# Kernel tuning notes

Hardware: AMD Instinct MI355X
Metric: run time of the kernel (lower is better)

## Reference

```python
import jax, jax.numpy as jnp
import numpy as np

B, N, D, H, L = 1024, 500, 128, 8, 2  # batch, nb_nodes, dim_emb, nb_heads, nb_layers_decoder
CLIP = 10.0


def _mha(q, K, V, h, mask, clip):
    # q: (B,1,D) single query; K,V: (B,N,D); mask: (B,N) True = forbidden
    Bsz, Nn, Dd = K.shape
    dh = Dd // h
    qh = q.reshape(Bsz, h, dh)            # head k takes contiguous chunk of dim_emb (matches torch view)
    Kh = K.reshape(Bsz, Nn, h, dh)
    Vh = V.reshape(Bsz, Nn, h, dh)
    scores = jnp.einsum('bhd,bnhd->bhn', qh, Kh) / jnp.sqrt(jnp.asarray(dh, q.dtype))
    if clip is not None:
        scores = clip * jnp.tanh(scores)
    scores = jnp.where(mask[:, None, :], jnp.asarray(-1e9, scores.dtype), scores)
    w = jax.nn.softmax(scores, axis=-1)   # (B,h,N)
    out = jnp.einsum('bhn,bnhd->bhd', w, Vh).reshape(Bsz, 1, Dd)
    return out, w.mean(axis=1, keepdims=True)  # (B,1,D), (B,1,N)


def setup_inputs() -> dict:
    key = jax.random.key(0)
    ks = jax.random.split(key, 8)
    query = jax.random.normal(ks[0], (B, 1, D), dtype=jnp.float32)
    K_att = jax.random.normal(ks[1], (B, N, D * L), dtype=jnp.float32)
    V_att = jax.random.normal(ks[2], (B, N, D * L), dtype=jnp.float32)
    mask = jax.random.bernoulli(ks[3], 0.3, (B, N))
    mask = mask.at[:, 0].set(False)  # guarantee every row has a legal action
    s = 1.0 / np.sqrt(D)
    W0_w = jax.random.normal(ks[4], (D, D), dtype=jnp.float32) * s
    W0_b = jnp.zeros((D,), dtype=jnp.float32)
    Wq_w = jax.random.normal(ks[5], (D, D), dtype=jnp.float32) * s
    Wq_b = jnp.zeros((D,), dtype=jnp.float32)
    return {"query": query, "K_att": K_att, "V_att": V_att, "mask": mask,
            "W0_w": W0_w, "W0_b": W0_b, "Wq_w": Wq_w, "Wq_b": Wq_b}


def reference(query, K_att, V_att, mask, W0_w, W0_b, Wq_w, Wq_b):
    q = query
    attn_w = None
    for l in range(L):
        Kl = K_att[:, :, l * D:(l + 1) * D]
        Vl = V_att[:, :, l * D:(l + 1) * D]
        if l < L - 1:
            out, _ = _mha(q, Kl, Vl, H, mask, None)
            q = out @ W0_w.T + W0_b
        else:
            qf = q @ Wq_w.T + Wq_b
            _, attn_w = _mha(qf, Kl, Vl, 1, mask, CLIP)
    return attn_w[:, 0, :]  # (B, N) prob of next node
```

## Files before the change

kernel.cpp:

```cpp
#include <hip/hip_runtime.h>
#include <hip/hip_bf16.h>
#include <math.h>

constexpr int NKEY = 500;
constexpr int DIM = 128;
constexpr int ROWSTRIDE = 256;

typedef __attribute__((ext_vector_type(4))) float f32x4;

__device__ __forceinline__ f32x4 nt_load4(const float* p) {
    return __builtin_nontemporal_load((const f32x4*)p);
}
__device__ __forceinline__ void nt_store(float* p, float v) {
    __builtin_nontemporal_store(v, p);
}
__device__ __forceinline__ float fast_tanh10(float x) {
    const float ax = fabsf(x);
    const float e = __expf(2.f * ax);
    const float r = 1.f - 2.f / (e + 1.f);
    return copysignf(10.f * r, x);
}

__global__ __launch_bounds__(256, 5)
void fused_pomo_attn(const float* __restrict__ query,
                     const float* __restrict__ K_att,
                     const float* __restrict__ V_att,
                     const int*   __restrict__ mask,
                     const float* __restrict__ W0_w,
                     const float* __restrict__ W0_b,
                     const float* __restrict__ Wq_w,
                     const float* __restrict__ Wq_b,
                     float* __restrict__ out)
{
    const int b = blockIdx.x;
    const int tid = threadIdx.x;
    const int lane32 = tid & 31;
    const int grp = tid >> 5;

    __shared__ alignas(16) float s_red[8][DIM];
    __shared__ float s_m8[8][32];
    __shared__ float s_l8[8][32];
    __shared__ alignas(16) float s_out[DIM];
    __shared__ alignas(16) float s_q1[DIM];
    __shared__ alignas(16) float s_qf[DIM];
    __shared__ alignas(16) float s_s1[NKEY];
    __shared__ int s_idx[NKEY];
    __shared__ int s_cnt;
    __shared__ float s_m[4], s_l[4];

    const size_t brow = (size_t)b * NKEY;

    if (tid < 64) {
        int off = 0;
        for (int base = 0; base < NKEY; base += 64) {
            const int n = base + tid;
            const bool keep = (n < NKEY) && (mask[brow + n] == 0);
            const unsigned long long bal = __ballot(keep);
            const int pre = __popcll(bal & ((1ull << tid) - 1ull));
            if (keep) s_idx[off + pre] = n;
            off += __popcll(bal);
        }
        if (tid == 0) s_cnt = off;
    }
    __syncthreads();
    const int M = s_cnt;
    const int Mm1 = M - 1;

    {
        const f32x4 q4 = ((const f32x4*)(query + (size_t)b * DIM))[lane32];
        const float* Kb = K_att + brow * ROWSTRIDE + lane32 * 4;
        const float* Vb = V_att + brow * ROWSTRIDE + lane32 * 4;
        float m = -1e30f, l = 0.f;
        f32x4 acc; acc[0]=0.f; acc[1]=0.f; acc[2]=0.f; acc[3]=0.f;
        for (int base = 0; base < M; base += 32) {
            int n[4]; bool okv[4];
            #pragma unroll
            for (int j = 0; j < 4; j++) {
                const int p = base + 8*j + grp;
                okv[j] = p < M;
                n[j] = s_idx[okv[j] ? p : Mm1];
            }
            f32x4 k[4], v[4];
            #pragma unroll
            for (int j = 0; j < 4; j++) k[j] = nt_load4(Kb + (size_t)n[j] * ROWSTRIDE);
            #pragma unroll
            for (int j = 0; j < 4; j++) v[j] = nt_load4(Vb + (size_t)n[j] * ROWSTRIDE);
            float s[4];
            #pragma unroll
            for (int j = 0; j < 4; j++)
                s[j] = q4[0]*k[j][0] + q4[1]*k[j][1] + q4[2]*k[j][2] + q4[3]*k[j][3];
            #pragma unroll
            for (int j = 0; j < 4; j++) { s[j] += __shfl_xor(s[j], 1); s[j] += __shfl_xor(s[j], 2); }
            #pragma unroll
            for (int j = 0; j < 4; j++) s[j] = okv[j] ? s[j] * 0.25f : -1e30f;
            float m2 = m;
            #pragma unroll
            for (int j = 0; j < 4; j++) m2 = fmaxf(m2, s[j]);
            const float f = __expf(m - m2);
            float w[4];
            #pragma unroll
            for (int j = 0; j < 4; j++) w[j] = __expf(s[j] - m2);
            l = l * f + (w[0] + w[1]) + (w[2] + w[3]);
            #pragma unroll
            for (int d = 0; d < 4; d++) {
                float a = acc[d] * f;
                #pragma unroll
                for (int j = 0; j < 4; j++) a += w[j] * v[j][d];
                acc[d] = a;
            }
            m = m2;
        }
        ((f32x4*)s_red[grp])[lane32] = acc;
        s_m8[grp][lane32] = m;
        s_l8[grp][lane32] = l;
    }
    __syncthreads();
    if (tid < DIM) {
        const int ql = tid >> 2;
        float M_ = -1e30f;
        #pragma unroll
        for (int g = 0; g < 8; g++) M_ = fmaxf(M_, s_m8[g][ql]);
        float L = 0.f, o = 0.f;
        #pragma unroll
        for (int g = 0; g < 8; g++) {
            const float f = __expf(s_m8[g][ql] - M_);
            L += s_l8[g][ql] * f;
            o += s_red[g][tid] * f;
        }
        s_out[tid] = o / L;
    }
    __syncthreads();

    {
        const int i = tid >> 1, half = tid & 1;
        const float4* wrow = (const float4*)(W0_w + (size_t)i * DIM + half * 64);
        float ssum = 0.f;
        #pragma unroll
        for (int k = 0; k < 16; k++) {
            const float4 w4 = wrow[k];
            const float4 o4 = ((const float4*)s_out)[half * 16 + k];
            ssum += w4.x*o4.x + w4.y*o4.y + w4.z*o4.z + w4.w*o4.w;
        }
        ssum += __shfl_xor(ssum, 1);
        if (half == 0) s_q1[i] = ssum + W0_b[i];
    }
    __syncthreads();

    {
        const int i = tid >> 1, half = tid & 1;
        const float4* wrow = (const float4*)(Wq_w + (size_t)i * DIM + half * 64);
        float ssum = 0.f;
        #pragma unroll
        for (int k = 0; k < 16; k++) {
            const float4 w4 = wrow[k];
            const float4 o4 = ((const float4*)s_q1)[half * 16 + k];
            ssum += w4.x*o4.x + w4.y*o4.y + w4.z*o4.z + w4.w*o4.w;
        }
        ssum += __shfl_xor(ssum, 1);
        if (half == 0) s_qf[i] = ssum + Wq_b[i];
    }
    __syncthreads();

    {
        const f32x4 qf4 = ((const f32x4*)s_qf)[lane32];
        const float* K1b = K_att + brow * ROWSTRIDE + DIM + lane32 * 4;
        f32x4 kt[4];
        #pragma unroll
        for (int j = 0; j < 4; j++) {
            const int p = 8*j + grp;
            const int nn = s_idx[p < M ? p : Mm1];
            kt[j] = nt_load4(K1b + (size_t)nn * ROWSTRIDE);
        }
        for (int base = 0; base < M; base += 32) {
            f32x4 kn[4];
            #pragma unroll
            for (int j = 0; j < 4; j++) {
                const int p = base + 32 + 8*j + grp;
                const int nn = s_idx[p < M ? p : Mm1];
                kn[j] = nt_load4(K1b + (size_t)nn * ROWSTRIDE);
            }
            float s[4];
            #pragma unroll
            for (int j = 0; j < 4; j++)
                s[j] = qf4[0]*kt[j][0] + qf4[1]*kt[j][1] + qf4[2]*kt[j][2] + qf4[3]*kt[j][3];
            #pragma unroll
            for (int o = 1; o < 32; o <<= 1) {
                #pragma unroll
                for (int j = 0; j < 4; j++) s[j] += __shfl_xor(s[j], o);
            }
            if (lane32 == 0) {
                #pragma unroll
                for (int j = 0; j < 4; j++) {
                    const int p = base + 8*j + grp;
                    if (p < M) s_s1[p] = fast_tanh10(s[j] * 0.08838834764831845f);
                }
            }
            #pragma unroll
            for (int j = 0; j < 4; j++) kt[j] = kn[j];
        }
    }
    for (int n = tid; n < NKEY; n += 256) nt_store(out + brow + n, 0.f);
    __syncthreads();

    {
        const int wid = tid >> 6;
        const int lane = tid & 63;
        float m = -INFINITY;
        for (int p = tid; p < M; p += 256) m = fmaxf(m, s_s1[p]);
        #pragma unroll
        for (int o = 32; o > 0; o >>= 1) m = fmaxf(m, __shfl_xor(m, o));
        if (lane == 0) s_m[wid] = m;
        __syncthreads();
        m = fmaxf(fmaxf(s_m[0], s_m[1]), fmaxf(s_m[2], s_m[3]));
        float l = 0.f;
        for (int p = tid; p < M; p += 256) {
            const float e = __expf(s_s1[p] - m);
            s_s1[p] = e;
            l += e;
        }
        #pragma unroll
        for (int o = 32; o > 0; o >>= 1) l += __shfl_xor(l, o);
        if (lane == 0) s_l[wid] = l;
        __syncthreads();
        l = s_l[0] + s_l[1] + s_l[2] + s_l[3];
        const float inv = 1.f / l;
        for (int p = tid; p < M; p += 256) nt_store(out + brow + s_idx[p], s_s1[p] * inv);
    }
}

extern "C" void kernel_launch(void* const* d_in, const int* in_sizes, int n_in,
                              void* d_out, int out_size, void* d_ws, size_t ws_size,
                              hipStream_t stream) {
    const float* query = (const float*)d_in[0];
    const float* K_att = (const float*)d_in[1];
    const float* V_att = (const float*)d_in[2];
    const int*   mask  = (const int*)d_in[3];
    const float* W0_w  = (const float*)d_in[4];
    const float* W0_b  = (const float*)d_in[5];
    const float* Wq_w  = (const float*)d_in[6];
    const float* Wq_b  = (const float*)d_in[7];
    float* out = (float*)d_out;

    const int B = in_sizes[0] / DIM;
    fused_pomo_attn<<<B, 256, 0, stream>>>(query, K_att, V_att, mask,
                                           W0_w, W0_b, Wq_w, Wq_b, out);
}
```

Before: 104.8 us.

## Parallelize mask compaction across waves and prefetch layer-1 keys earlier

Mask compaction now runs across all four waves, using per-wave ballot counts and a prefix sum instead of one wave looping eight times. The first 64 gathered K rows of the second layer are loaded right after the first attention pass, so their latency overlaps the reduction and the two small matvecs. The score loop now prefetches two tiles ahead. Holding the extra prefetch registers required lowering the occupancy hint from 5 to 4 blocks per SM, which reduces latency hiding across blocks.

Result: no change. 106.1 us (+1.2%).

```diff
diff --git a/kernel.cpp b/kernel.cpp
--- a/kernel.cpp
+++ b/kernel.cpp
@@ -21,7 +21,7 @@
     return copysignf(10.f * r, x);
 }
 
-__global__ __launch_bounds__(256, 5)
+__global__ __launch_bounds__(256, 4)
 void fused_pomo_attn(const float* __restrict__ query,
                      const float* __restrict__ K_att,
                      const float* __restrict__ V_att,
@@ -45,25 +45,34 @@
     __shared__ alignas(16) float s_qf[DIM];
     __shared__ alignas(16) float s_s1[NKEY];
     __shared__ int s_idx[NKEY];
-    __shared__ int s_cnt;
+    __shared__ int s_wcnt[4];
     __shared__ float s_m[4], s_l[4];
 
     const size_t brow = (size_t)b * NKEY;
 
-    if (tid < 64) {
-        int off = 0;
-        for (int base = 0; base < NKEY; base += 64) {
-            const int n = base + tid;
-            const bool keep = (n < NKEY) && (mask[brow + n] == 0);
-            const unsigned long long bal = __ballot(keep);
-            const int pre = __popcll(bal & ((1ull << tid) - 1ull));
-            if (keep) s_idx[off + pre] = n;
-            off += __popcll(bal);
-        }
-        if (tid == 0) s_cnt = off;
-    }
-    __syncthreads();
-    const int M = s_cnt;
+    {
+        const int cwid = tid >> 6;
+        const int cwl  = tid & 63;
+        const int kstart = cwid * 128;
+        const int kend   = min(kstart + 128, NKEY);
+        const int n0 = kstart + cwl;
+        const int n1 = kstart + 64 + cwl;
+        const bool keep0 = (n0 < kend) && (mask[brow + n0] == 0);
+        const bool keep1 = (n1 < kend) && (mask[brow + n1] == 0);
+        const unsigned long long b0 = __ballot(keep0);
+        const unsigned long long b1 = __ballot(keep1);
+        const int c0 = __popcll(b0);
+        if (cwl == 0) s_wcnt[cwid] = c0 + __popcll(b1);
+        __syncthreads();
+        int pref = 0;
+        #pragma unroll
+        for (int w = 0; w < 4; w++) if (w < cwid) pref += s_wcnt[w];
+        const unsigned long long mlow = (1ull << cwl) - 1ull;
+        if (keep0) s_idx[pref + __popcll(b0 & mlow)] = n0;
+        if (keep1) s_idx[pref + c0 + __popcll(b1 & mlow)] = n1;
+    }
+    __syncthreads();
+    const int M = s_wcnt[0] + s_wcnt[1] + s_wcnt[2] + s_wcnt[3];
     const int Mm1 = M - 1;
 
     {
@@ -115,6 +124,20 @@
         s_l8[grp][lane32] = l;
     }
     __syncthreads();
+
+    const float* K1b = K_att + brow * ROWSTRIDE + DIM + lane32 * 4;
+    f32x4 kA[4], kB[4];
+    #pragma unroll
+    for (int j = 0; j < 4; j++) {
+        const int p = 8*j + grp;
+        kA[j] = nt_load4(K1b + (size_t)s_idx[p < M ? p : Mm1] * ROWSTRIDE);
+    }
+    #pragma unroll
+    for (int j = 0; j < 4; j++) {
+        const int p = 32 + 8*j + grp;
+        kB[j] = nt_load4(K1b + (size_t)s_idx[p < M ? p : Mm1] * ROWSTRIDE);
+    }
+
     if (tid < DIM) {
         const int ql = tid >> 2;
         float M_ = -1e30f;
@@ -163,26 +186,18 @@
 
     {
         const f32x4 qf4 = ((const f32x4*)s_qf)[lane32];
-        const float* K1b = K_att + brow * ROWSTRIDE + DIM + lane32 * 4;
-        f32x4 kt[4];
-        #pragma unroll
-        for (int j = 0; j < 4; j++) {
-            const int p = 8*j + grp;
-            const int nn = s_idx[p < M ? p : Mm1];
-            kt[j] = nt_load4(K1b + (size_t)nn * ROWSTRIDE);
-        }
         for (int base = 0; base < M; base += 32) {
-            f32x4 kn[4];
+            float s[4];
+            #pragma unroll
+            for (int j = 0; j < 4; j++)
+                s[j] = qf4[0]*kA[j][0] + qf4[1]*kA[j][1] + qf4[2]*kA[j][2] + qf4[3]*kA[j][3];
+            #pragma unroll
+            for (int j = 0; j < 4; j++) kA[j] = kB[j];
             #pragma unroll
             for (int j = 0; j < 4; j++) {
-                const int p = base + 32 + 8*j + grp;
-                const int nn = s_idx[p < M ? p : Mm1];
-                kn[j] = nt_load4(K1b + (size_t)nn * ROWSTRIDE);
-            }
-            float s[4];
-            #pragma unroll
-            for (int j = 0; j < 4; j++)
-                s[j] = qf4[0]*kt[j][0] + qf4[1]*kt[j][1] + qf4[2]*kt[j][2] + qf4[3]*kt[j][3];
+                const int p = base + 64 + 8*j + grp;
+                kB[j] = nt_load4(K1b + (size_t)s_idx[p < M ? p : Mm1] * ROWSTRIDE);
+            }
             #pragma unroll
             for (int o = 1; o < 32; o <<= 1) {
                 #pragma unroll
@@ -195,8 +210,6 @@
                     if (p < M) s_s1[p] = fast_tanh10(s[j] * 0.08838834764831845f);
                 }
             }
-            #pragma unroll
-            for (int j = 0; j < 4; j++) kt[j] = kn[j];
         }
     }
     for (int n = tid; n < NKEY; n += 256) nt_store(out + brow + n, 0.f);
```
